# Kernel optimization log

Measured on AMD Instinct MI355X. Metric: run time of the kernel, lower is better.

Reference implementation:

```python
import jax, jax.numpy as jnp
from jax import lax
import numpy as np

EMA_ALPHA = 0.3
LN_EPS = 1e-5
SW = 5  # center_window_size


def _gelu(x):
    return jax.nn.gelu(x, approximate=False)  # torch nn.GELU default = exact erf


def _layernorm(x, g, b):
    mu = x.mean(-1, keepdims=True)
    var = ((x - mu) ** 2).mean(-1, keepdims=True)
    return (x - mu) * lax.rsqrt(var + LN_EPS) * g + b


def _ema_scan(x, alpha):
    # x: [B, T, C]; x_smooth[t] = lerp(x_smooth[t-1], x[t], alpha)
    x0 = x[:, 0]
    def step(prev, xt):
        s = prev + alpha * (xt - prev)
        return s, s
    _, ys = lax.scan(step, x0, jnp.swapaxes(x[:, 1:], 0, 1))  # [T-1, B, C]
    return jnp.concatenate([x0[:, None], jnp.swapaxes(ys, 0, 1)], axis=1)


def _lstm_dir(x, w_ih, w_hh, b):
    # x: [B, T, Cin]; w_ih: [Cin, 4H]; w_hh: [H, 4H]; b: [4H]. torch gate order i,f,g,o
    B = x.shape[0]
    H = w_hh.shape[0]
    pre = jnp.einsum('btc,ch->bth', x, w_ih) + b  # [B, T, 4H]
    def step(carry, p):
        h, c = carry
        gates = p + h @ w_hh
        i, f, g, o = jnp.split(gates, 4, axis=-1)
        c = jax.nn.sigmoid(f) * c + jax.nn.sigmoid(i) * jnp.tanh(g)
        h = jax.nn.sigmoid(o) * jnp.tanh(c)
        return (h, c), h
    init = (jnp.zeros((B, H), x.dtype), jnp.zeros((B, H), x.dtype))
    _, hs = lax.scan(step, init, jnp.swapaxes(pre, 0, 1))  # [T, B, H]
    return jnp.swapaxes(hs, 0, 1)


def _bilstm(x, wih_f, whh_f, b_f, wih_r, whh_r, b_r):
    fwd = _lstm_dir(x, wih_f, whh_f, b_f)
    bwd = jnp.flip(_lstm_dir(jnp.flip(x, axis=1), wih_r, whh_r, b_r), axis=1)
    return jnp.concatenate([fwd, bwd], axis=-1)  # [B, T, 2H]


def setup_inputs() -> dict:
    key = jax.random.key(0)
    ks = jax.random.split(key, 24)
    B, T, C, BD, O, H = 4096, 31, 768, 128, 12, 64
    AUG = 3 * BD  # 384
    def n(k, shape, s):
        return jax.random.normal(k, shape, dtype=jnp.float32) * s
    return {
        'x': n(ks[0], (B, T, C), 1.0),
        'cls_w': n(ks[1], (C, BD), 0.03), 'cls_b': jnp.zeros((BD,), jnp.float32),
        'delta_w': n(ks[2], (C, BD), 0.03), 'delta_b': jnp.zeros((BD,), jnp.float32),
        'acc_w': n(ks[3], (C, BD), 0.03), 'acc_b': jnp.zeros((BD,), jnp.float32),
        'cls_ln_g': jnp.ones((BD,), jnp.float32), 'cls_ln_b': jnp.zeros((BD,), jnp.float32),
        'delta_ln_g': jnp.ones((BD,), jnp.float32), 'delta_ln_b': jnp.zeros((BD,), jnp.float32),
        'acc_ln_g': jnp.ones((BD,), jnp.float32), 'acc_ln_b': jnp.zeros((BD,), jnp.float32),
        'lin0_w': n(ks[4], (AUG, 256), 0.05), 'lin0_b': jnp.zeros((256,), jnp.float32),
        'gate': jnp.float32(0.2),
        'attn_w': n(ks[5], (2 * H, 1), 0.08), 'attn_b': jnp.zeros((1,), jnp.float32),
        'attn_temp': jnp.float32(1.0),
        'lin1_w': n(ks[6], (C, O), 0.03), 'lin1_b': jnp.zeros((O,), jnp.float32),
        'lin2_w': n(ks[7], (2 * H, O), 0.08), 'lin2_b': jnp.zeros((O,), jnp.float32),
        'lstm_wih_f': n(ks[8], (256, 4 * H), 0.06), 'lstm_whh_f': n(ks[9], (H, 4 * H), 0.12),
        'lstm_b_f': jnp.zeros((4 * H,), jnp.float32),
        'lstm_wih_r': n(ks[10], (256, 4 * H), 0.06), 'lstm_whh_r': n(ks[11], (H, 4 * H), 0.12),
        'lstm_b_r': jnp.zeros((4 * H,), jnp.float32),
    }


def reference(x, cls_w, cls_b, delta_w, delta_b, acc_w, acc_b,
              cls_ln_g, cls_ln_b, delta_ln_g, delta_ln_b, acc_ln_g, acc_ln_b,
              lin0_w, lin0_b, gate, attn_w, attn_b, attn_temp,
              lin1_w, lin1_b, lin2_w, lin2_b,
              lstm_wih_f, lstm_whh_f, lstm_b_f, lstm_wih_r, lstm_whh_r, lstm_b_r):
    T = x.shape[1]
    hsl = T // 2
    l, r = max(0, hsl - SW), min(T, hsl + SW + 1)  # center window [10, 21) for T=31

    # --- robust deltas: EMA smoothing + reflect-padded finite differences ---
    x_smooth = _ema_scan(x, EMA_ALPHA)                       # [B, T, C]
    padded = jnp.pad(x_smooth, ((0, 0), (2, 0), (0, 0)), mode='reflect')  # [B, T+2, C]
    dx = padded[:, 1:] - padded[:, :-1]                       # [B, T+1, C]
    ddx = dx[:, 1:] - dx[:, :-1]                              # [B, T, C]
    delta_stream = dx[:, 1:]                                  # [B, T, C]
    acc_stream = ddx                                          # [B, T, C]

    # --- linear branch: mean of lin1 over center window of smoothed stream ---
    linear_logits = (x_smooth[:, l:r] @ lin1_w + lin1_b).mean(axis=1)  # [B, O]

    # --- bottlenecks (eval mode: dropout identity) + LayerNorms ---
    cls_bn = _layernorm(_gelu(x_smooth @ cls_w + cls_b), cls_ln_g, cls_ln_b)
    delta_bn = _layernorm(_gelu(delta_stream @ delta_w + delta_b), delta_ln_g, delta_ln_b)
    acc_bn = _layernorm(_gelu(acc_stream @ acc_w + acc_b), acc_ln_g, acc_ln_b)
    x_aug = jnp.concatenate([cls_bn, delta_bn, acc_bn], axis=-1)  # [B, T, 384]

    x_lstm = _gelu(x_aug @ lin0_w + lin0_b)                   # [B, T, 256]
    x_lstm = x_lstm - x_lstm.mean(axis=1, keepdims=True)      # center over time (fp32)

    # --- BiLSTM + attention pooling over center window ---
    lstm_out = _bilstm(x_lstm, lstm_wih_f, lstm_whh_f, lstm_b_f,
                       lstm_wih_r, lstm_whh_r, lstm_b_r)      # [B, T, 128]
    window = lstm_out[:, l:r]                                 # [B, W, 128]
    temp = jax.nn.softplus(attn_temp) + 0.001
    scores = (window @ attn_w + attn_b)[..., 0] / temp        # [B, W]
    attn = jax.nn.softmax(scores, axis=1)[..., None]          # [B, W, 1]
    attended = (attn * window).sum(axis=1)                    # [B, 128]
    lstm_logits = attended @ lin2_w + lin2_b                  # [B, O]

    g = jax.nn.sigmoid(gate)
    final_logits = linear_logits + g * (lstm_logits - linear_logits)
    return final_logits, attended
```

## Files before the change

### kernel.cpp

```cpp
#include <hip/hip_runtime.h>
#include <cstdint>
#include <cstddef>


typedef short s8v __attribute__((ext_vector_type(8)));
typedef float f4v __attribute__((ext_vector_type(4)));

#if defined(__has_builtin)
#if __has_builtin(__builtin_amdgcn_global_load_lds)
#define HAVE_GLL 1
#endif
#endif
#ifndef HAVE_GLL
#define HAVE_GLL 0
#endif

__device__ __forceinline__ unsigned short f2bf(float f) {
  union { float f; unsigned int u; } v; v.f = f;
  unsigned int u = v.u;
  return (unsigned short)((u + 0x7fffu + ((u >> 16) & 1u)) >> 16);
}
__device__ __forceinline__ float bf2f(unsigned short h) {
  union { unsigned int u; float f; } v; v.u = ((unsigned int)h) << 16;
  return v.f;
}
__device__ __forceinline__ float fsig(float x) {
  return __fdividef(1.f, 1.f + __expf(-x));
}
__device__ __forceinline__ float ftanh(float x) {
  return 1.f - __fdividef(2.f, 1.f + __expf(2.f * x));
}
__device__ __forceinline__ float fgelu(float x) {
  return 0.5f * x * (1.f + erff(x * 0.70710678118654752f));
}

__device__ __forceinline__ void ld_lds16(const unsigned short* g,
                                         unsigned short* ldsU, int lane) {
#if HAVE_GLL
  __builtin_amdgcn_global_load_lds(
      (__attribute__((address_space(1))) void*)(uintptr_t)(const void*)g,
      (__attribute__((address_space(3))) void*)(unsigned int)(uintptr_t)(void*)ldsU,
      16, 0, 0);
#else
  *(uint4*)(ldsU + lane * 8) = *(const uint4*)g;
#endif
}
__device__ __forceinline__ void wait_vm0() {
#if HAVE_GLL
  __builtin_amdgcn_s_waitcnt(0x0F70);
#endif
}

#define OFF_W1T   0u
#define OFF_W2T   589824u
#define OFF_WIHT  786432u
#define OFF_WHHT  1048576u
#define OFF_XS    1114112u
#define OFF_XW    196149248u
#define OFF_LL    208732160u
#define OFF_WIN   208928768u
#define OFF_XAUG  220463104u
#define OFF_XLSTM 317980672u

__global__ __launch_bounds__(256) void k0_prep(
    const float* __restrict__ cls_w, const float* __restrict__ delta_w,
    const float* __restrict__ acc_w, const float* __restrict__ lin0_w,
    const float* __restrict__ wih_f, const float* __restrict__ wih_r,
    const float* __restrict__ whh_f, const float* __restrict__ whh_r,
    unsigned short* __restrict__ ws) {
  int i = blockIdx.x * 256 + threadIdx.x;
  if (i < 294912) {
    int n = i / 768, k = i - n * 768;
    int seg = n >> 7, nn = n & 127;
    const float* w = seg == 0 ? cls_w : (seg == 1 ? delta_w : acc_w);
    ws[i] = f2bf(w[k * 128 + nn]);
  } else if (i < 393216) {
    int j = i - 294912;
    int n = j / 384, k = j - n * 384;
    ws[i] = f2bf(lin0_w[k * 256 + n]);
  } else if (i < 524288) {
    int j = i - 393216;
    int n = j >> 8, k = j & 255;
    ws[i] = f2bf(n < 256 ? wih_f[k * 256 + n] : wih_r[k * 256 + (n - 256)]);
  } else if (i < 557056) {
    int j = i - 524288;
    int d = j >> 14, rem = j & 16383;
    int n = rem >> 6, k = rem & 63;
    const float* w = d ? whh_r : whh_f;
    ws[i] = f2bf(w[k * 256 + n]);
  }
}

__global__ __launch_bounds__(256) void k1_ema(
    const float* __restrict__ x, unsigned short* __restrict__ xs,
    float* __restrict__ xw) {
  int gid = blockIdx.x * 256 + threadIdx.x;
  int b = gid / 768;
  int c = gid - b * 768;
  size_t base = (size_t)b * 31 * 768 + c;
  float s = x[base];
  xs[base] = f2bf(s);
  float wsum = 0.f;
#pragma unroll
  for (int t = 1; t < 31; ++t) {
    float xv = x[base + t * 768];
    s = s + 0.3f * (xv - s);
    xs[base + t * 768] = f2bf(s);
    if (t >= 10 && t <= 20) wsum += s;
  }
  xw[gid] = wsum * (1.f / 11.f);
}

__global__ __launch_bounds__(64) void k1b_linlog(
    const float* __restrict__ xw, const float* __restrict__ lin1_w,
    const float* __restrict__ lin1_b, float* __restrict__ ll) {
  int b = blockIdx.x;
  int lane = threadIdx.x;
  float p[12];
#pragma unroll
  for (int o = 0; o < 12; ++o) p[o] = 0.f;
  for (int k = lane; k < 768; k += 64) {
    float xv = xw[b * 768 + k];
    const float* w = lin1_w + k * 12;
#pragma unroll
    for (int o = 0; o < 12; ++o) p[o] += xv * w[o];
  }
#pragma unroll
  for (int o = 0; o < 12; ++o) {
    float v = p[o];
#pragma unroll
    for (int s = 1; s < 64; s <<= 1) v += __shfl_xor(v, s, 64);
    p[o] = v;
  }
  if (lane == 0) {
#pragma unroll
    for (int o = 0; o < 12; ++o) ll[b * 12 + o] = p[o] + lin1_b[o];
  }
}

template <int KDIM>
__device__ __forceinline__ void gemm128(
    const unsigned short* __restrict__ A, int rowClamp,
    const unsigned short* __restrict__ Bt,
    unsigned short* sA, unsigned short* sB, f4v acc[4][4]) {
  const int tid  = threadIdx.x;
  const int lane = tid & 63;
  const int wv   = tid >> 6;
  const int l15  = lane & 15;
  const int quad = lane >> 4;
  const int mh   = (wv >> 1) * 64;
  const int nh   = (wv & 1) * 64;

  const int srow = wv * 32 + (lane >> 3);
  const int scol = (lane & 7) * 8;
  const unsigned short* aBase[4];
  const unsigned short* bBase[4];
  unsigned short* aDst[4];
  unsigned short* bDst[4];
#pragma unroll
  for (int j = 0; j < 4; ++j) {
    int r = srow + j * 8;
    int ar = r < rowClamp ? r : rowClamp;
    aBase[j] = A + (size_t)ar * KDIM + scol;
    bBase[j] = Bt + (size_t)r * KDIM + scol;
    aDst[j] = sA + (wv * 4 + j) * 512;
    bDst[j] = sB + (wv * 4 + j) * 512;
  }
#pragma unroll
  for (int mt = 0; mt < 4; ++mt)
#pragma unroll
    for (int nt = 0; nt < 4; ++nt)
      acc[mt][nt] = (f4v){0.f, 0.f, 0.f, 0.f};

  constexpr int KT = KDIM / 64;
  for (int kt = 0; kt < KT; ++kt) {
    if (kt) __syncthreads();
    int ko = kt * 64;
#pragma unroll
    for (int j = 0; j < 4; ++j) ld_lds16(aBase[j] + ko, aDst[j], lane);
#pragma unroll
    for (int j = 0; j < 4; ++j) ld_lds16(bBase[j] + ko, bDst[j], lane);
    wait_vm0();
    __syncthreads();
#pragma unroll
    for (int ks = 0; ks < 2; ++ks) {
      s8v af[4], bfv[4];
#pragma unroll
      for (int mt = 0; mt < 4; ++mt)
        af[mt] = *(const s8v*)(&sA[(mh + mt * 16 + l15) * 64 + ks * 32 + quad * 8]);
#pragma unroll
      for (int nt = 0; nt < 4; ++nt)
        bfv[nt] = *(const s8v*)(&sB[(nh + nt * 16 + l15) * 64 + ks * 32 + quad * 8]);
#pragma unroll
      for (int mt = 0; mt < 4; ++mt)
#pragma unroll
        for (int nt = 0; nt < 4; ++nt)
          acc[mt][nt] = __builtin_amdgcn_mfma_f32_16x16x32_bf16(af[mt], bfv[nt], acc[mt][nt], 0, 0, 0);
    }
  }
  __syncthreads();
}

__device__ __forceinline__ void dump_chunk(f4v acc[4][4], float* sP, int lo,
                                           int nrows, int pstr) {
  const int tid  = threadIdx.x;
  const int lane = tid & 63;
  const int wv   = tid >> 6;
  const int l15  = lane & 15;
  const int quad = lane >> 4;
  const int mh   = (wv >> 1) * 64;
  const int nh   = (wv & 1) * 64;
#pragma unroll
  for (int mt = 0; mt < 4; ++mt)
#pragma unroll
    for (int nt = 0; nt < 4; ++nt)
#pragma unroll
      for (int r = 0; r < 4; ++r) {
        int rr = mh + mt * 16 + quad * 4 + r - lo;
        if ((unsigned)rr < (unsigned)nrows)
          sP[rr * pstr + nh + nt * 16 + l15] = acc[mt][nt][r];
      }
}

__device__ __forceinline__ float stencil_gelu3(const float* sP, const float* sBias,
                                               int seg, int t, int c) {
  const float* p = sP + t * 390 + seg * 130 + c;
  float v;
  if (seg == 0) {
    v = p[0];
  } else if (seg == 1) {
    v = (t == 0) ? (p[0] - p[390]) : (p[0] - p[-390]);
  } else {
    if (t == 0)      v = p[0] - 2.f * p[390] + p[780];
    else if (t == 1) v = 2.f * (p[0] - p[-390]);
    else             v = p[0] - 2.f * p[-390] + p[-780];
  }
  return fgelu(v + sBias[seg * 128 + c]);
}

__global__ __launch_bounds__(1024) void k2_aug(
    const unsigned short* __restrict__ xs, const unsigned short* __restrict__ W1t,
    const float* __restrict__ cls_b, const float* __restrict__ delta_b,
    const float* __restrict__ acc_b,
    const float* __restrict__ g0, const float* __restrict__ be0,
    const float* __restrict__ g1, const float* __restrict__ be1,
    const float* __restrict__ g2, const float* __restrict__ be2,
    unsigned short* __restrict__ xaug) {
  __shared__ __align__(16) char smem[131072];
  unsigned short* buf0 = (unsigned short*)smem;
  unsigned short* buf1 = (unsigned short*)(smem + 65536);
  float* sP    = (float*)smem;
  float* sBias = (float*)(smem + 65536);
  float* sG    = sBias + 384;
  float* sLb   = sG + 384;
  float* sMu   = sLb + 384;
  float* sRs   = sMu + 93;

  const int tid  = threadIdx.x;
  const int lane = tid & 63;
  const int wv   = tid >> 6;
  const int l15  = lane & 15;
  const int quad = lane >> 4;
  const int wm   = wv >> 3;
  const int wn   = wv & 7;
  const int rowBase = blockIdx.x * 124;

  const int subrow = lane >> 3;
  const int schunk = ((lane & 7) ^ subrow) * 8;
  const unsigned short* src[4];
#pragma unroll
  for (int j = 0; j < 4; ++j) {
    int slice = wv * 4 + j;
    int row = slice * 8 + subrow;
    src[j] = (row < 128)
        ? xs + (size_t)(rowBase + (row < 124 ? row : 123)) * 768 + schunk
        : W1t + (size_t)(row - 128) * 768 + schunk;
  }

  f4v acc[4][3];
#pragma unroll
  for (int mt = 0; mt < 4; ++mt)
#pragma unroll
    for (int nt = 0; nt < 3; ++nt) acc[mt][nt] = (f4v){0.f, 0.f, 0.f, 0.f};

  const int swz = (l15 & 7) << 3;

#pragma unroll
  for (int j = 0; j < 4; ++j) ld_lds16(src[j], buf0 + (wv * 4 + j) * 512, lane);
  wait_vm0();
  __syncthreads();

  for (int kt = 0; kt < 12; ++kt) {
    unsigned short* bc = (kt & 1) ? buf1 : buf0;
    unsigned short* bn = (kt & 1) ? buf0 : buf1;
    if (kt < 11) {
#pragma unroll
      for (int j = 0; j < 4; ++j)
        ld_lds16(src[j] + (kt + 1) * 64, bn + (wv * 4 + j) * 512, lane);
    }
#pragma unroll
    for (int ks = 0; ks < 2; ++ks) {
      s8v af[4], bfv[3];
      const int ko = (ks * 32 + quad * 8) ^ swz;
#pragma unroll
      for (int mt = 0; mt < 4; ++mt)
        af[mt] = *(const s8v*)(&bc[(wm * 64 + mt * 16 + l15) * 64 + ko]);
#pragma unroll
      for (int nt = 0; nt < 3; ++nt)
        bfv[nt] = *(const s8v*)(&bc[(128 + wn * 48 + nt * 16 + l15) * 64 + ko]);
#pragma unroll
      for (int mt = 0; mt < 4; ++mt)
#pragma unroll
        for (int nt = 0; nt < 3; ++nt)
          acc[mt][nt] = __builtin_amdgcn_mfma_f32_16x16x32_bf16(af[mt], bfv[nt], acc[mt][nt], 0, 0, 0);
    }
    wait_vm0();
    __syncthreads();
  }

  if (tid < 384) {
    int seg = tid >> 7, c = tid & 127;
    sBias[tid] = seg == 0 ? cls_b[c] : (seg == 1 ? delta_b[c] : acc_b[c]);
    sG[tid]    = seg == 0 ? g0[c]    : (seg == 1 ? g1[c]    : g2[c]);
    sLb[tid]   = seg == 0 ? be0[c]   : (seg == 1 ? be1[c]   : be2[c]);
  }

#pragma unroll
  for (int ck = 0; ck < 4; ++ck) {
    int lo = ck * 31;
#pragma unroll
    for (int mt = 0; mt < 4; ++mt) {
      int rbase = wm * 64 + mt * 16 + quad * 4 - lo;
#pragma unroll
      for (int nt = 0; nt < 3; ++nt) {
        int gcol = wn * 48 + nt * 16;
        int colp = (gcol >> 7) * 130 + (gcol & 127) + l15;
#pragma unroll
        for (int r = 0; r < 4; ++r) {
          int rr = rbase + r;
          if ((unsigned)rr < 31u) sP[rr * 390 + colp] = acc[mt][nt][r];
        }
      }
    }
    __syncthreads();
    if (tid < 744) {
      int seg = tid < 248 ? 0 : (tid < 496 ? 1 : 2);
      int rem = tid - seg * 248;
      int row = rem >> 3, q = rem & 7;
      float sum = 0.f, ss = 0.f;
#pragma unroll
      for (int i = 0; i < 16; ++i) {
        float v = stencil_gelu3(sP, sBias, seg, row, q + 8 * i);
        sum += v; ss += v * v;
      }
      sum += __shfl_xor(sum, 1, 64); ss += __shfl_xor(ss, 1, 64);
      sum += __shfl_xor(sum, 2, 64); ss += __shfl_xor(ss, 2, 64);
      sum += __shfl_xor(sum, 4, 64); ss += __shfl_xor(ss, 4, 64);
      if (q == 0) {
        float mu = sum * (1.f / 128.f);
        sMu[seg * 31 + row] = mu;
        sRs[seg * 31 + row] = rsqrtf(ss * (1.f / 128.f) - mu * mu + 1e-5f);
      }
    }
    __syncthreads();
#pragma unroll
    for (int seg = 0; seg < 3; ++seg) {
      for (int idx = tid; idx < 31 * 128; idx += 1024) {
        int row = idx >> 7, c = idx & 127;
        float v = stencil_gelu3(sP, sBias, seg, row, c);
        float o = (v - sMu[seg * 31 + row]) * sRs[seg * 31 + row]
                  * sG[seg * 128 + c] + sLb[seg * 128 + c];
        xaug[(size_t)(rowBase + lo + row) * 384 + seg * 128 + c] = f2bf(o);
      }
    }
    __syncthreads();
  }
}

__global__ __launch_bounds__(256) void k3_lstm_in(
    const unsigned short* __restrict__ xaug, const unsigned short* __restrict__ W2t,
    const float* __restrict__ lin0_b, unsigned short* __restrict__ xlstm) {
  __shared__ __align__(16) char smem[33792];
  unsigned short* sA = (unsigned short*)smem;
  unsigned short* sB = (unsigned short*)(smem + 16384);
  float* sP  = (float*)smem;
  float* sCM = (float*)(smem + 32768);
  int by = blockIdx.y;
  int rowBase = blockIdx.x * 124;
  f4v acc[4][4];
  gemm128<384>(xaug + (size_t)rowBase * 384, 123, W2t + (size_t)by * 128 * 384, sA, sB, acc);
  int tid = threadIdx.x;
#pragma unroll
  for (int ck = 0; ck < 2; ++ck) {
    int lo = ck * 62;
    dump_chunk(acc, sP, lo, 62, 132);
    __syncthreads();
    for (int idx = tid; idx < 62 * 128; idx += 256) {
      int row = idx >> 7, col = idx & 127;
      sP[row * 132 + col] = fgelu(sP[row * 132 + col] + lin0_b[by * 128 + col]);
    }
    __syncthreads();
    {
      int bb = tid >> 7, col = tid & 127;
      float s = 0.f;
      for (int tr = 0; tr < 31; ++tr) s += sP[(bb * 31 + tr) * 132 + col];
      sCM[tid] = s * (1.f / 31.f);
    }
    __syncthreads();
    for (int idx = tid; idx < 62 * 128; idx += 256) {
      int row = idx >> 7, col = idx & 127;
      int bb = row >= 31 ? 1 : 0;
      float v = sP[row * 132 + col] - sCM[bb * 128 + col];
      xlstm[(size_t)(rowBase + lo + row) * 256 + by * 128 + col] = f2bf(v);
    }
    __syncthreads();
  }
}

__global__ __launch_bounds__(256) void k3b_pre(
    const unsigned short* __restrict__ xlstm, const unsigned short* __restrict__ Wiht,
    const float* __restrict__ b_f, const float* __restrict__ b_r,
    unsigned short* __restrict__ pre) {
  __shared__ __align__(16) char smem[32768];
  unsigned short* sA = (unsigned short*)smem;
  unsigned short* sB = (unsigned short*)(smem + 16384);
  float* sP = (float*)smem;
  int by = blockIdx.y;
  int rowBase = blockIdx.x * 128;
  f4v acc[4][4];
  gemm128<256>(xlstm + (size_t)rowBase * 256, 127, Wiht + (size_t)by * 128 * 256, sA, sB, acc);
  int tid = threadIdx.x;
#pragma unroll
  for (int ck = 0; ck < 2; ++ck) {
    int lo = ck * 64;
    dump_chunk(acc, sP, lo, 64, 128);
    __syncthreads();
    for (int idx = tid; idx < 64 * 128; idx += 256) {
      int row = idx >> 7, col = idx & 127;
      int gcol = by * 128 + col;
      float bias = gcol < 256 ? b_f[gcol] : b_r[gcol - 256];
      pre[(size_t)(rowBase + lo + row) * 512 + gcol] = f2bf(sP[row * 128 + col] + bias);
    }
    __syncthreads();
  }
}

__global__ __launch_bounds__(256) void k4_lstm(
    const unsigned short* __restrict__ pre, const unsigned short* __restrict__ Whht,
    unsigned short* __restrict__ win) {
  __shared__ unsigned short sW[256 * 72];
  __shared__ unsigned short sH[16 * 72];
  __shared__ float sG[16 * 260];
  int tid = threadIdx.x;
  int dir = blockIdx.y;
  int b0  = blockIdx.x * 16;
  {
    const unsigned short* src = Whht + dir * 16384;
#pragma unroll
    for (int c = 0; c < 8; ++c) {
      int id = tid + c * 256;
      int row = id >> 3, kc = (id & 7) * 8;
      uint4 v = *(const uint4*)(src + row * 64 + kc);
      *(uint4*)(&sW[row * 72 + kc]) = v;
    }
  }
  for (int i = tid; i < 16 * 72; i += 256) sH[i] = 0;
  __syncthreads();

  const int lane = tid & 63, wv = tid >> 6, l15 = lane & 15, quad = lane >> 4;
  const int eb = tid >> 4, jb = (tid & 15) * 4;
  float cs[4] = {0.f, 0.f, 0.f, 0.f};

  int tt0 = dir ? 30 : 0;
  const unsigned short* pbase = pre + ((size_t)(b0 + eb) * 31) * 512 + dir * 256;
  ushort4 pi = *(const ushort4*)(pbase + tt0 * 512 + jb);
  ushort4 pf = *(const ushort4*)(pbase + tt0 * 512 + 64 + jb);
  ushort4 pg = *(const ushort4*)(pbase + tt0 * 512 + 128 + jb);
  ushort4 po = *(const ushort4*)(pbase + tt0 * 512 + 192 + jb);

  for (int t = 0; t < 31; ++t) {
    f4v acc[4];
#pragma unroll
    for (int nt = 0; nt < 4; ++nt) acc[nt] = (f4v){0.f, 0.f, 0.f, 0.f};
#pragma unroll
    for (int ks = 0; ks < 2; ++ks) {
      s8v af = *(const s8v*)(&sH[l15 * 72 + ks * 32 + quad * 8]);
#pragma unroll
      for (int nt = 0; nt < 4; ++nt) {
        int n = wv * 64 + nt * 16 + l15;
        s8v bfv = *(const s8v*)(&sW[n * 72 + ks * 32 + quad * 8]);
        acc[nt] = __builtin_amdgcn_mfma_f32_16x16x32_bf16(af, bfv, acc[nt], 0, 0, 0);
      }
    }
#pragma unroll
    for (int nt = 0; nt < 4; ++nt)
#pragma unroll
      for (int r = 0; r < 4; ++r)
        sG[(quad * 4 + r) * 260 + wv * 64 + nt * 16 + l15] = acc[nt][r];

    ushort4 ni, nf, ng, no;
    if (t < 30) {
      int ttn = dir ? 29 - t : t + 1;
      ni = *(const ushort4*)(pbase + ttn * 512 + jb);
      nf = *(const ushort4*)(pbase + ttn * 512 + 64 + jb);
      ng = *(const ushort4*)(pbase + ttn * 512 + 128 + jb);
      no = *(const ushort4*)(pbase + ttn * 512 + 192 + jb);
    }
    __syncthreads();

    int tt = dir ? 30 - t : t;
    const float* g = &sG[eb * 260];
    float hv[4];
#pragma unroll
    for (int jj = 0; jj < 4; ++jj) {
      int j = jb + jj;
      float vi = g[j]       + bf2f(jj == 0 ? pi.x : jj == 1 ? pi.y : jj == 2 ? pi.z : pi.w);
      float vf = g[64 + j]  + bf2f(jj == 0 ? pf.x : jj == 1 ? pf.y : jj == 2 ? pf.z : pf.w);
      float vg = g[128 + j] + bf2f(jj == 0 ? pg.x : jj == 1 ? pg.y : jj == 2 ? pg.z : pg.w);
      float vo = g[192 + j] + bf2f(jj == 0 ? po.x : jj == 1 ? po.y : jj == 2 ? po.z : po.w);
      float cc = fsig(vf) * cs[jj] + fsig(vi) * ftanh(vg);
      cs[jj] = cc;
      hv[jj] = fsig(vo) * ftanh(cc);
    }
    ushort4 hb;
    hb.x = f2bf(hv[0]); hb.y = f2bf(hv[1]); hb.z = f2bf(hv[2]); hb.w = f2bf(hv[3]);
    *(ushort4*)(&sH[eb * 72 + jb]) = hb;
    if (tt >= 10 && tt <= 20)
      *(ushort4*)(win + ((size_t)(b0 + eb) * 11 + (tt - 10)) * 128 + dir * 64 + jb) = hb;
    if (t < 30) { pi = ni; pf = nf; pg = ng; po = no; }
    __syncthreads();
  }
}

__global__ __launch_bounds__(256) void k5_attn(
    const unsigned short* __restrict__ win, const float* __restrict__ attn_w,
    const float* __restrict__ attn_b, const float* __restrict__ attn_t,
    const float* __restrict__ lin2_w, const float* __restrict__ lin2_b,
    const float* __restrict__ linlog, const float* __restrict__ gate,
    float* __restrict__ out) {
  __shared__ unsigned short sWin[176 * 128];
  __shared__ float sAw[128];
  __shared__ float sSc[176];
  __shared__ float sAtt[16 * 128];
  int tid = threadIdx.x;
  int b0  = blockIdx.x * 16;
#pragma unroll
  for (int c = 0; c < 11; ++c) {
    int id = tid + c * 256;
    int row = id >> 4, kc = (id & 15) * 8;
    uint4 v = *(const uint4*)(win + ((size_t)b0 * 11 + row) * 128 + kc);
    *(uint4*)(&sWin[row * 128 + kc]) = v;
  }
  if (tid < 128) sAw[tid] = attn_w[tid];
  __syncthreads();
  if (tid < 176) {
    int b = tid / 11, wt = tid - b * 11;
    const unsigned short* w = &sWin[(b * 11 + wt) * 128];
    float dot = 0.f;
    for (int ch = 0; ch < 128; ++ch) dot += bf2f(w[ch]) * sAw[ch];
    float temp = logf(1.f + __expf(attn_t[0])) + 0.001f;
    sSc[tid] = (dot + attn_b[0]) / temp;
  }
  __syncthreads();
  if (tid < 16) {
    float m = -1e30f;
    for (int wt = 0; wt < 11; ++wt) m = fmaxf(m, sSc[tid * 11 + wt]);
    float e[11], sum = 0.f;
    for (int wt = 0; wt < 11; ++wt) { e[wt] = __expf(sSc[tid * 11 + wt] - m); sum += e[wt]; }
    float inv = __fdividef(1.f, sum);
    for (int wt = 0; wt < 11; ++wt) sSc[tid * 11 + wt] = e[wt] * inv;
  }
  __syncthreads();
#pragma unroll
  for (int p = 0; p < 8; ++p) {
    int task = tid + p * 256;
    int b = task >> 7, ch = task & 127;
    float a = 0.f;
    for (int wt = 0; wt < 11; ++wt)
      a += sSc[b * 11 + wt] * bf2f(sWin[(b * 11 + wt) * 128 + ch]);
    sAtt[b * 128 + ch] = a;
    out[49152 + (size_t)(b0 + b) * 128 + ch] = a;
  }
  __syncthreads();
  if (tid < 192) {
    int b = tid / 12, o = tid - b * 12;
    float dot = 0.f;
    for (int ch = 0; ch < 128; ++ch) dot += sAtt[b * 128 + ch] * lin2_w[ch * 12 + o];
    dot += lin2_b[o];
    float lin = linlog[(size_t)(b0 + b) * 12 + o];
    float gg = fsig(gate[0]);
    out[(size_t)(b0 + b) * 12 + o] = lin + gg * (dot - lin);
  }
}

extern "C" void kernel_launch(void* const* d_in, const int* in_sizes, int n_in,
                              void* d_out, int out_size, void* d_ws, size_t ws_size,
                              hipStream_t stream) {
  const float* x       = (const float*)d_in[0];
  const float* cls_w   = (const float*)d_in[1];
  const float* cls_b   = (const float*)d_in[2];
  const float* delta_w = (const float*)d_in[3];
  const float* delta_b = (const float*)d_in[4];
  const float* acc_w   = (const float*)d_in[5];
  const float* acc_b   = (const float*)d_in[6];
  const float* cls_g   = (const float*)d_in[7];
  const float* cls_be  = (const float*)d_in[8];
  const float* del_g   = (const float*)d_in[9];
  const float* del_be  = (const float*)d_in[10];
  const float* accg    = (const float*)d_in[11];
  const float* accbe   = (const float*)d_in[12];
  const float* lin0_w  = (const float*)d_in[13];
  const float* lin0_b  = (const float*)d_in[14];
  const float* gate    = (const float*)d_in[15];
  const float* attn_w  = (const float*)d_in[16];
  const float* attn_b  = (const float*)d_in[17];
  const float* attn_t  = (const float*)d_in[18];
  const float* lin1_w  = (const float*)d_in[19];
  const float* lin1_b  = (const float*)d_in[20];
  const float* lin2_w  = (const float*)d_in[21];
  const float* lin2_b  = (const float*)d_in[22];
  const float* wih_f   = (const float*)d_in[23];
  const float* whh_f   = (const float*)d_in[24];
  const float* b_f     = (const float*)d_in[25];
  const float* wih_r   = (const float*)d_in[26];
  const float* whh_r   = (const float*)d_in[27];
  const float* b_r     = (const float*)d_in[28];

  char* ws = (char*)d_ws;
  unsigned short* W1t   = (unsigned short*)(ws + OFF_W1T);
  unsigned short* W2t   = (unsigned short*)(ws + OFF_W2T);
  unsigned short* Wiht  = (unsigned short*)(ws + OFF_WIHT);
  unsigned short* Whht  = (unsigned short*)(ws + OFF_WHHT);
  unsigned short* XS    = (unsigned short*)(ws + OFF_XS);
  unsigned short* PRE   = XS;
  float*          XW    = (float*)(ws + OFF_XW);
  float*          LL    = (float*)(ws + OFF_LL);
  unsigned short* WIN   = (unsigned short*)(ws + OFF_WIN);
  unsigned short* XAUG  = (unsigned short*)(ws + OFF_XAUG);
  unsigned short* XLSTM = (unsigned short*)(ws + OFF_XLSTM);
  float* out = (float*)d_out;

  k0_prep<<<2176, 256, 0, stream>>>(cls_w, delta_w, acc_w, lin0_w, wih_f, wih_r,
                                    whh_f, whh_r, (unsigned short*)ws);
  k1_ema<<<12288, 256, 0, stream>>>(x, XS, XW);
  k1b_linlog<<<4096, 64, 0, stream>>>(XW, lin1_w, lin1_b, LL);
  k2_aug<<<1024, 1024, 0, stream>>>(XS, W1t, cls_b, delta_b, acc_b,
                                    cls_g, cls_be, del_g, del_be, accg, accbe, XAUG);
  k3_lstm_in<<<dim3(1024, 2), 256, 0, stream>>>(XAUG, W2t, lin0_b, XLSTM);
  k3b_pre<<<dim3(992, 4), 256, 0, stream>>>(XLSTM, Wiht, b_f, b_r, PRE);
  k4_lstm<<<dim3(256, 2), 256, 0, stream>>>(PRE, Whht, WIN);
  k5_attn<<<256, 256, 0, stream>>>(WIN, attn_w, attn_b, attn_t, lin2_w, lin2_b,
                                   LL, gate, out);
}
```

Baseline: 1.101 ms.

## Fuse lin0 GEMM, centering and LSTM input projection into one kernel

Merges the lin0+GELU+time-centering kernel and the LSTM input-projection kernel into a single 1024-thread kernel. The centered activations stay in LDS instead of round-tripping through global memory. The GEMM tiles are double-buffered with XOR-swizzled LDS layouts so loads overlap MFMA work. The EMA kernel is also changed to process two channels per thread with float2 loads and packed bf16 stores. The fused kernel needs about 132KB of LDS and 1024 threads per block, which limits occupancy to one block per CU.

```diff
diff --git a/kernel.cpp b/kernel.cpp
--- a/kernel.cpp
+++ b/kernel.cpp
@@ -60,7 +60,6 @@
 #define OFF_LL    208732160u
 #define OFF_WIN   208928768u
 #define OFF_XAUG  220463104u
-#define OFF_XLSTM 317980672u
 
 __global__ __launch_bounds__(256) void k0_prep(
     const float* __restrict__ cls_w, const float* __restrict__ delta_w,
@@ -95,20 +94,24 @@
     const float* __restrict__ x, unsigned short* __restrict__ xs,
     float* __restrict__ xw) {
   int gid = blockIdx.x * 256 + threadIdx.x;
-  int b = gid / 768;
-  int c = gid - b * 768;
-  size_t base = (size_t)b * 31 * 768 + c;
-  float s = x[base];
-  xs[base] = f2bf(s);
-  float wsum = 0.f;
+  int b = gid / 384;
+  int cp = gid - b * 384;
+  size_t base = (size_t)b * 31 * 768 + cp * 2;
+  float2 s = *(const float2*)(x + base);
+  *(unsigned int*)(xs + base) =
+      (unsigned int)f2bf(s.x) | ((unsigned int)f2bf(s.y) << 16);
+  float w0 = 0.f, w1 = 0.f;
 #pragma unroll
   for (int t = 1; t < 31; ++t) {
-    float xv = x[base + t * 768];
-    s = s + 0.3f * (xv - s);
-    xs[base + t * 768] = f2bf(s);
-    if (t >= 10 && t <= 20) wsum += s;
-  }
-  xw[gid] = wsum * (1.f / 11.f);
+    float2 xv = *(const float2*)(x + base + t * 768);
+    s.x += 0.3f * (xv.x - s.x);
+    s.y += 0.3f * (xv.y - s.y);
+    *(unsigned int*)(xs + base + t * 768) =
+        (unsigned int)f2bf(s.x) | ((unsigned int)f2bf(s.y) << 16);
+    if (t >= 10 && t <= 20) { w0 += s.x; w1 += s.y; }
+  }
+  float2 wm; wm.x = w0 * (1.f / 11.f); wm.y = w1 * (1.f / 11.f);
+  *(float2*)(xw + (size_t)b * 768 + cp * 2) = wm;
 }
 
 __global__ __launch_bounds__(64) void k1b_linlog(
@@ -136,90 +139,6 @@
 #pragma unroll
     for (int o = 0; o < 12; ++o) ll[b * 12 + o] = p[o] + lin1_b[o];
   }
-}
-
-template <int KDIM>
-__device__ __forceinline__ void gemm128(
-    const unsigned short* __restrict__ A, int rowClamp,
-    const unsigned short* __restrict__ Bt,
-    unsigned short* sA, unsigned short* sB, f4v acc[4][4]) {
-  const int tid  = threadIdx.x;
-  const int lane = tid & 63;
-  const int wv   = tid >> 6;
-  const int l15  = lane & 15;
-  const int quad = lane >> 4;
-  const int mh   = (wv >> 1) * 64;
-  const int nh   = (wv & 1) * 64;
-
-  const int srow = wv * 32 + (lane >> 3);
-  const int scol = (lane & 7) * 8;
-  const unsigned short* aBase[4];
-  const unsigned short* bBase[4];
-  unsigned short* aDst[4];
-  unsigned short* bDst[4];
-#pragma unroll
-  for (int j = 0; j < 4; ++j) {
-    int r = srow + j * 8;
-    int ar = r < rowClamp ? r : rowClamp;
-    aBase[j] = A + (size_t)ar * KDIM + scol;
-    bBase[j] = Bt + (size_t)r * KDIM + scol;
-    aDst[j] = sA + (wv * 4 + j) * 512;
-    bDst[j] = sB + (wv * 4 + j) * 512;
-  }
-#pragma unroll
-  for (int mt = 0; mt < 4; ++mt)
-#pragma unroll
-    for (int nt = 0; nt < 4; ++nt)
-      acc[mt][nt] = (f4v){0.f, 0.f, 0.f, 0.f};
-
-  constexpr int KT = KDIM / 64;
-  for (int kt = 0; kt < KT; ++kt) {
-    if (kt) __syncthreads();
-    int ko = kt * 64;
-#pragma unroll
-    for (int j = 0; j < 4; ++j) ld_lds16(aBase[j] + ko, aDst[j], lane);
-#pragma unroll
-    for (int j = 0; j < 4; ++j) ld_lds16(bBase[j] + ko, bDst[j], lane);
-    wait_vm0();
-    __syncthreads();
-#pragma unroll
-    for (int ks = 0; ks < 2; ++ks) {
-      s8v af[4], bfv[4];
-#pragma unroll
-      for (int mt = 0; mt < 4; ++mt)
-        af[mt] = *(const s8v*)(&sA[(mh + mt * 16 + l15) * 64 + ks * 32 + quad * 8]);
-#pragma unroll
-      for (int nt = 0; nt < 4; ++nt)
-        bfv[nt] = *(const s8v*)(&sB[(nh + nt * 16 + l15) * 64 + ks * 32 + quad * 8]);
-#pragma unroll
-      for (int mt = 0; mt < 4; ++mt)
-#pragma unroll
-        for (int nt = 0; nt < 4; ++nt)
-          acc[mt][nt] = __builtin_amdgcn_mfma_f32_16x16x32_bf16(af[mt], bfv[nt], acc[mt][nt], 0, 0, 0);
-    }
-  }
-  __syncthreads();
-}
-
-__device__ __forceinline__ void dump_chunk(f4v acc[4][4], float* sP, int lo,
-                                           int nrows, int pstr) {
-  const int tid  = threadIdx.x;
-  const int lane = tid & 63;
-  const int wv   = tid >> 6;
-  const int l15  = lane & 15;
-  const int quad = lane >> 4;
-  const int mh   = (wv >> 1) * 64;
-  const int nh   = (wv & 1) * 64;
-#pragma unroll
-  for (int mt = 0; mt < 4; ++mt)
-#pragma unroll
-    for (int nt = 0; nt < 4; ++nt)
-#pragma unroll
-      for (int r = 0; r < 4; ++r) {
-        int rr = mh + mt * 16 + quad * 4 + r - lo;
-        if ((unsigned)rr < (unsigned)nrows)
-          sP[rr * pstr + nh + nt * 16 + l15] = acc[mt][nt][r];
-      }
 }
 
 __device__ __forceinline__ float stencil_gelu3(const float* sP, const float* sBias,
@@ -377,71 +296,191 @@
   }
 }
 
-__global__ __launch_bounds__(256) void k3_lstm_in(
+__global__ __launch_bounds__(1024) void k3c_fused(
     const unsigned short* __restrict__ xaug, const unsigned short* __restrict__ W2t,
-    const float* __restrict__ lin0_b, unsigned short* __restrict__ xlstm) {
-  __shared__ __align__(16) char smem[33792];
-  unsigned short* sA = (unsigned short*)smem;
-  unsigned short* sB = (unsigned short*)(smem + 16384);
-  float* sP  = (float*)smem;
-  float* sCM = (float*)(smem + 32768);
-  int by = blockIdx.y;
-  int rowBase = blockIdx.x * 124;
-  f4v acc[4][4];
-  gemm128<384>(xaug + (size_t)rowBase * 384, 123, W2t + (size_t)by * 128 * 384, sA, sB, acc);
-  int tid = threadIdx.x;
-#pragma unroll
-  for (int ck = 0; ck < 2; ++ck) {
-    int lo = ck * 62;
-    dump_chunk(acc, sP, lo, 62, 132);
-    __syncthreads();
-    for (int idx = tid; idx < 62 * 128; idx += 256) {
-      int row = idx >> 7, col = idx & 127;
-      sP[row * 132 + col] = fgelu(sP[row * 132 + col] + lin0_b[by * 128 + col]);
-    }
-    __syncthreads();
-    {
-      int bb = tid >> 7, col = tid & 127;
-      float s = 0.f;
-      for (int tr = 0; tr < 31; ++tr) s += sP[(bb * 31 + tr) * 132 + col];
-      sCM[tid] = s * (1.f / 31.f);
-    }
-    __syncthreads();
-    for (int idx = tid; idx < 62 * 128; idx += 256) {
-      int row = idx >> 7, col = idx & 127;
-      int bb = row >= 31 ? 1 : 0;
-      float v = sP[row * 132 + col] - sCM[bb * 128 + col];
-      xlstm[(size_t)(rowBase + lo + row) * 256 + by * 128 + col] = f2bf(v);
-    }
-    __syncthreads();
-  }
-}
-
-__global__ __launch_bounds__(256) void k3b_pre(
-    const unsigned short* __restrict__ xlstm, const unsigned short* __restrict__ Wiht,
+    const unsigned short* __restrict__ Wiht, const float* __restrict__ lin0_b,
     const float* __restrict__ b_f, const float* __restrict__ b_r,
     unsigned short* __restrict__ pre) {
-  __shared__ __align__(16) char smem[32768];
-  unsigned short* sA = (unsigned short*)smem;
-  unsigned short* sB = (unsigned short*)(smem + 16384);
-  float* sP = (float*)smem;
-  int by = blockIdx.y;
-  int rowBase = blockIdx.x * 128;
-  f4v acc[4][4];
-  gemm128<256>(xlstm + (size_t)rowBase * 256, 127, Wiht + (size_t)by * 128 * 256, sA, sB, acc);
-  int tid = threadIdx.x;
-#pragma unroll
-  for (int ck = 0; ck < 2; ++ck) {
-    int lo = ck * 64;
-    dump_chunk(acc, sP, lo, 64, 128);
-    __syncthreads();
-    for (int idx = tid; idx < 64 * 128; idx += 256) {
-      int row = idx >> 7, col = idx & 127;
-      int gcol = by * 128 + col;
-      float bias = gcol < 256 ? b_f[gcol] : b_r[gcol - 256];
-      pre[(size_t)(rowBase + lo + row) * 512 + gcol] = f2bf(sP[row * 128 + col] + bias);
-    }
-    __syncthreads();
+  __shared__ __align__(16) char smem[135168];
+  unsigned short* stg2  = (unsigned short*)smem;
+  unsigned short* xlstm = (unsigned short*)smem;
+  unsigned short* stg3  = (unsigned short*)(smem + 65536);
+  unsigned short* sPb   = (unsigned short*)(smem + 65536);
+  float*          sP2   = (float*)(smem + 98304);
+  float* sL0b = (float*)(smem + 131072);
+  float* sB3  = sL0b + 256;
+  float* sCM  = sB3 + 512;
+
+  const int tid  = threadIdx.x;
+  const int lane = tid & 63;
+  const int wv   = tid >> 6;
+  const int l15  = lane & 15;
+  const int quad = lane >> 4;
+  const int wm   = wv >> 3;
+  const int wn   = wv & 7;
+  const int rowBase = blockIdx.x * 124;
+
+  if (tid < 256) sL0b[tid] = lin0_b[tid];
+  else if (tid < 768) {
+    int i = tid - 256;
+    sB3[i] = i < 256 ? b_f[i] : b_r[i - 256];
+  }
+
+  const int subrow  = lane >> 3;
+  const int schunk8 = ((lane & 7) ^ subrow) * 8;
+  const int swz     = (l15 & 7) << 3;
+
+  const unsigned short* src2[3];
+#pragma unroll
+  for (int j = 0; j < 3; ++j) {
+    int row = (wv * 3 + j) * 8 + subrow;
+    src2[j] = (row < 128)
+        ? xaug + (size_t)(rowBase + (row < 124 ? row : 123)) * 384 + schunk8
+        : W2t + (size_t)(row - 128) * 384 + schunk8;
+  }
+  f4v acc2[4][2];
+#pragma unroll
+  for (int mt = 0; mt < 4; ++mt)
+#pragma unroll
+    for (int nt = 0; nt < 2; ++nt) acc2[mt][nt] = (f4v){0.f, 0.f, 0.f, 0.f};
+
+#pragma unroll
+  for (int j = 0; j < 3; ++j) ld_lds16(src2[j], stg2 + (wv * 3 + j) * 512, lane);
+  wait_vm0();
+  __syncthreads();
+
+  for (int kt = 0; kt < 6; ++kt) {
+    unsigned short* bc = stg2 + (kt & 1) * 24576;
+    unsigned short* bn = stg2 + ((kt & 1) ^ 1) * 24576;
+    if (kt < 5) {
+#pragma unroll
+      for (int j = 0; j < 3; ++j)
+        ld_lds16(src2[j] + (kt + 1) * 64, bn + (wv * 3 + j) * 512, lane);
+    }
+#pragma unroll
+    for (int ks = 0; ks < 2; ++ks) {
+      const int ko = (ks * 32 + quad * 8) ^ swz;
+      s8v af[4], bfv[2];
+#pragma unroll
+      for (int mt = 0; mt < 4; ++mt)
+        af[mt] = *(const s8v*)(&bc[(wm * 64 + mt * 16 + l15) * 64 + ko]);
+#pragma unroll
+      for (int nt = 0; nt < 2; ++nt)
+        bfv[nt] = *(const s8v*)(&bc[(128 + wn * 32 + nt * 16 + l15) * 64 + ko]);
+#pragma unroll
+      for (int mt = 0; mt < 4; ++mt)
+#pragma unroll
+        for (int nt = 0; nt < 2; ++nt)
+          acc2[mt][nt] = __builtin_amdgcn_mfma_f32_16x16x32_bf16(af[mt], bfv[nt], acc2[mt][nt], 0, 0, 0);
+    }
+    wait_vm0();
+    __syncthreads();
+  }
+
+  for (int ck = 0; ck < 4; ++ck) {
+    const int lo = ck * 31;
+#pragma unroll
+    for (int mt = 0; mt < 4; ++mt) {
+      int rbase = wm * 64 + mt * 16 + quad * 4 - lo;
+#pragma unroll
+      for (int nt = 0; nt < 2; ++nt) {
+        int col = wn * 32 + nt * 16 + l15;
+#pragma unroll
+        for (int r = 0; r < 4; ++r) {
+          int rr = rbase + r;
+          if ((unsigned)rr < 31u) sP2[rr * 260 + col] = acc2[mt][nt][r];
+        }
+      }
+    }
+    __syncthreads();
+    for (int idx = tid; idx < 31 * 256; idx += 1024) {
+      int row = idx >> 8, col = idx & 255;
+      sP2[row * 260 + col] = fgelu(sP2[row * 260 + col] + sL0b[col]);
+    }
+    __syncthreads();
+    if (tid < 256) {
+      float s = 0.f;
+      for (int tr = 0; tr < 31; ++tr) s += sP2[tr * 260 + tid];
+      sCM[tid] = s * (1.f / 31.f);
+    }
+    __syncthreads();
+    for (int idx = tid; idx < 31 * 128; idx += 1024) {
+      int row = idx >> 7, cp = (idx & 127) * 2;
+      float v0 = sP2[row * 260 + cp]     - sCM[cp];
+      float v1 = sP2[row * 260 + cp + 1] - sCM[cp + 1];
+      unsigned int u = (unsigned int)f2bf(v0) | ((unsigned int)f2bf(v1) << 16);
+      *(unsigned int*)(&xlstm[(size_t)(lo + row) * 260 + cp]) = u;
+    }
+    __syncthreads();
+  }
+
+  for (int p = 0; p < 2; ++p) {
+    const unsigned short* src3[2];
+#pragma unroll
+    for (int j = 0; j < 2; ++j) {
+      int row = (wv * 2 + j) * 8 + subrow;
+      src3[j] = Wiht + (size_t)(p * 256 + row) * 256 + schunk8;
+    }
+    f4v acc3[4][2];
+#pragma unroll
+    for (int mt = 0; mt < 4; ++mt)
+#pragma unroll
+      for (int nt = 0; nt < 2; ++nt) acc3[mt][nt] = (f4v){0.f, 0.f, 0.f, 0.f};
+#pragma unroll
+    for (int j = 0; j < 2; ++j) ld_lds16(src3[j], stg3 + (wv * 2 + j) * 512, lane);
+    wait_vm0();
+    __syncthreads();
+    for (int kt = 0; kt < 4; ++kt) {
+      unsigned short* bc = stg3 + (kt & 1) * 16384;
+      unsigned short* bn = stg3 + ((kt & 1) ^ 1) * 16384;
+      if (kt < 3) {
+#pragma unroll
+        for (int j = 0; j < 2; ++j)
+          ld_lds16(src3[j] + (kt + 1) * 64, bn + (wv * 2 + j) * 512, lane);
+      }
+#pragma unroll
+      for (int ks = 0; ks < 2; ++ks) {
+        const int ko = (ks * 32 + quad * 8) ^ swz;
+        s8v af[4], bfv[2];
+#pragma unroll
+        for (int mt = 0; mt < 4; ++mt)
+          af[mt] = *(const s8v*)(&xlstm[(size_t)(wm * 64 + mt * 16 + l15) * 260 + kt * 64 + ks * 32 + quad * 8]);
+#pragma unroll
+        for (int nt = 0; nt < 2; ++nt)
+          bfv[nt] = *(const s8v*)(&bc[(wn * 32 + nt * 16 + l15) * 64 + ko]);
+#pragma unroll
+        for (int mt = 0; mt < 4; ++mt)
+#pragma unroll
+          for (int nt = 0; nt < 2; ++nt)
+            acc3[mt][nt] = __builtin_amdgcn_mfma_f32_16x16x32_bf16(af[mt], bfv[nt], acc3[mt][nt], 0, 0, 0);
+      }
+      wait_vm0();
+      __syncthreads();
+    }
+    for (int ck = 0; ck < 4; ++ck) {
+      const int lo = ck * 31;
+#pragma unroll
+      for (int mt = 0; mt < 4; ++mt) {
+        int rbase = wm * 64 + mt * 16 + quad * 4 - lo;
+#pragma unroll
+        for (int nt = 0; nt < 2; ++nt) {
+          int col = wn * 32 + nt * 16 + l15;
+          float bias = sB3[p * 256 + col];
+#pragma unroll
+          for (int r = 0; r < 4; ++r) {
+            int rr = rbase + r;
+            if ((unsigned)rr < 31u) sPb[rr * 264 + col] = f2bf(acc3[mt][nt][r] + bias);
+          }
+        }
+      }
+      __syncthreads();
+      if (tid < 992) {
+        int row = tid >> 5, cq = (tid & 31) * 8;
+        *(uint4*)(pre + (size_t)(rowBase + lo + row) * 512 + p * 256 + cq) =
+            *(const uint4*)(&sPb[row * 264 + cq]);
+      }
+      __syncthreads();
+    }
   }
 }
 
@@ -637,17 +676,15 @@
   float*          LL    = (float*)(ws + OFF_LL);
   unsigned short* WIN   = (unsigned short*)(ws + OFF_WIN);
   unsigned short* XAUG  = (unsigned short*)(ws + OFF_XAUG);
-  unsigned short* XLSTM = (unsigned short*)(ws + OFF_XLSTM);
   float* out = (float*)d_out;
 
   k0_prep<<<2176, 256, 0, stream>>>(cls_w, delta_w, acc_w, lin0_w, wih_f, wih_r,
                                     whh_f, whh_r, (unsigned short*)ws);
-  k1_ema<<<12288, 256, 0, stream>>>(x, XS, XW);
+  k1_ema<<<6144, 256, 0, stream>>>(x, XS, XW);
   k1b_linlog<<<4096, 64, 0, stream>>>(XW, lin1_w, lin1_b, LL);
   k2_aug<<<1024, 1024, 0, stream>>>(XS, W1t, cls_b, delta_b, acc_b,
                                     cls_g, cls_be, del_g, del_be, accg, accbe, XAUG);
-  k3_lstm_in<<<dim3(1024, 2), 256, 0, stream>>>(XAUG, W2t, lin0_b, XLSTM);
-  k3b_pre<<<dim3(992, 4), 256, 0, stream>>>(XLSTM, Wiht, b_f, b_r, PRE);
+  k3c_fused<<<1024, 1024, 0, stream>>>(XAUG, W2t, Wiht, lin0_b, b_f, b_r, PRE);
   k4_lstm<<<dim3(256, 2), 256, 0, stream>>>(PRE, Whht, WIN);
   k5_attn<<<256, 256, 0, stream>>>(WIN, attn_w, attn_b, attn_t, lin2_w, lin2_b,
                                    LL, gate, out);
```

New measurement: 1.180 ms. 1.07x slower.

## Restructure LSTM recurrence to per-wave batches and vectorize EMA loads

Applied to the files above, without the earlier changes.

The LSTM kernel now gives each wavefront its own 16-row batch and has it compute all 256 gate columns. Gate nonlinearities are applied directly on MFMA accumulators, which removes the shared gate buffer and both block-wide barriers per timestep. The hidden state is exchanged through a per-wave LDS slot with only a waitcnt, and the precomputed input gates seed the accumulators. Separately, the EMA kernel processes four channels per thread with float4 loads, cutting its grid by four. In exchange, the LSTM uses more registers per thread (16 accumulators plus prefetch buffers), which can lower occupancy, and it launches half as many blocks of 128 threads.

```diff
diff --git a/kernel.cpp b/kernel.cpp
--- a/kernel.cpp
+++ b/kernel.cpp
@@ -95,20 +95,27 @@
     const float* __restrict__ x, unsigned short* __restrict__ xs,
     float* __restrict__ xw) {
   int gid = blockIdx.x * 256 + threadIdx.x;
-  int b = gid / 768;
-  int c = gid - b * 768;
-  size_t base = (size_t)b * 31 * 768 + c;
-  float s = x[base];
-  xs[base] = f2bf(s);
-  float wsum = 0.f;
+  int b = gid / 192;
+  int cq = gid - b * 192;
+  size_t base = (size_t)b * 31 * 768 + cq * 4;
+  float4 s = *(const float4*)(x + base);
+  ushort4 o;
+  o.x = f2bf(s.x); o.y = f2bf(s.y); o.z = f2bf(s.z); o.w = f2bf(s.w);
+  *(ushort4*)(xs + base) = o;
+  float w0 = 0.f, w1 = 0.f, w2 = 0.f, w3 = 0.f;
 #pragma unroll
   for (int t = 1; t < 31; ++t) {
-    float xv = x[base + t * 768];
-    s = s + 0.3f * (xv - s);
-    xs[base + t * 768] = f2bf(s);
-    if (t >= 10 && t <= 20) wsum += s;
-  }
-  xw[gid] = wsum * (1.f / 11.f);
+    float4 xv = *(const float4*)(x + base + t * 768);
+    s.x += 0.3f * (xv.x - s.x); s.y += 0.3f * (xv.y - s.y);
+    s.z += 0.3f * (xv.z - s.z); s.w += 0.3f * (xv.w - s.w);
+    o.x = f2bf(s.x); o.y = f2bf(s.y); o.z = f2bf(s.z); o.w = f2bf(s.w);
+    *(ushort4*)(xs + base + t * 768) = o;
+    if (t >= 10 && t <= 20) { w0 += s.x; w1 += s.y; w2 += s.z; w3 += s.w; }
+  }
+  float4 wm;
+  wm.x = w0 * (1.f / 11.f); wm.y = w1 * (1.f / 11.f);
+  wm.z = w2 * (1.f / 11.f); wm.w = w3 * (1.f / 11.f);
+  *(float4*)(xw + (size_t)b * 768 + cq * 4) = wm;
 }
 
 __global__ __launch_bounds__(64) void k1b_linlog(
@@ -445,90 +452,111 @@
   }
 }
 
-__global__ __launch_bounds__(256) void k4_lstm(
+__global__ __launch_bounds__(128) void k4_lstm(
     const unsigned short* __restrict__ pre, const unsigned short* __restrict__ Whht,
     unsigned short* __restrict__ win) {
   __shared__ unsigned short sW[256 * 72];
-  __shared__ unsigned short sH[16 * 72];
-  __shared__ float sG[16 * 260];
-  int tid = threadIdx.x;
-  int dir = blockIdx.y;
-  int b0  = blockIdx.x * 16;
+  __shared__ unsigned short sH[2][16 * 72];
+  const int tid  = threadIdx.x;
+  const int dir  = blockIdx.x & 1;
+  const int bg   = blockIdx.x >> 1;
+  const int wv   = tid >> 6;
+  const int lane = tid & 63;
+  const int l15  = lane & 15;
+  const int quad = lane >> 4;
+  const int b0   = bg * 32 + wv * 16;
+
   {
     const unsigned short* src = Whht + dir * 16384;
-#pragma unroll
-    for (int c = 0; c < 8; ++c) {
-      int id = tid + c * 256;
+    for (int id = tid; id < 2048; id += 128) {
       int row = id >> 3, kc = (id & 7) * 8;
-      uint4 v = *(const uint4*)(src + row * 64 + kc);
-      *(uint4*)(&sW[row * 72 + kc]) = v;
-    }
-  }
-  for (int i = tid; i < 16 * 72; i += 256) sH[i] = 0;
+      *(uint4*)(&sW[row * 72 + kc]) = *(const uint4*)(src + row * 64 + kc);
+    }
+  }
+  for (int i = lane; i < 16 * 72; i += 64) sH[wv][i] = 0;
   __syncthreads();
 
-  const int lane = tid & 63, wv = tid >> 6, l15 = lane & 15, quad = lane >> 4;
-  const int eb = tid >> 4, jb = (tid & 15) * 4;
-  float cs[4] = {0.f, 0.f, 0.f, 0.f};
-
-  int tt0 = dir ? 30 : 0;
-  const unsigned short* pbase = pre + ((size_t)(b0 + eb) * 31) * 512 + dir * 256;
-  ushort4 pi = *(const ushort4*)(pbase + tt0 * 512 + jb);
-  ushort4 pf = *(const ushort4*)(pbase + tt0 * 512 + 64 + jb);
-  ushort4 pg = *(const ushort4*)(pbase + tt0 * 512 + 128 + jb);
-  ushort4 po = *(const ushort4*)(pbase + tt0 * 512 + 192 + jb);
+  const unsigned short* pb[4];
+#pragma unroll
+  for (int r = 0; r < 4; ++r)
+    pb[r] = pre + ((size_t)(b0 + quad * 4 + r) * 31) * 512 + dir * 256 + l15;
+
+  float cs[4][4];
+#pragma unroll
+  for (int nt = 0; nt < 4; ++nt)
+#pragma unroll
+    for (int r = 0; r < 4; ++r) cs[nt][r] = 0.f;
+
+  s8v hf0 = {0, 0, 0, 0, 0, 0, 0, 0};
+  s8v hf1 = {0, 0, 0, 0, 0, 0, 0, 0};
+
+  unsigned short pcur[16][4];
+  {
+    const int tt0 = dir ? 30 : 0;
+#pragma unroll
+    for (int nt = 0; nt < 16; ++nt)
+#pragma unroll
+      for (int r = 0; r < 4; ++r)
+        pcur[nt][r] = pb[r][(size_t)tt0 * 512 + nt * 16];
+  }
 
   for (int t = 0; t < 31; ++t) {
-    f4v acc[4];
-#pragma unroll
-    for (int nt = 0; nt < 4; ++nt) acc[nt] = (f4v){0.f, 0.f, 0.f, 0.f};
+    const int tt = dir ? 30 - t : t;
+    f4v acc[16];
+#pragma unroll
+    for (int nt = 0; nt < 16; ++nt)
+#pragma unroll
+      for (int r = 0; r < 4; ++r) acc[nt][r] = bf2f(pcur[nt][r]);
+
+    unsigned short pnext[16][4];
+    if (t < 30) {
+      const int ttn = dir ? 29 - t : t + 1;
+#pragma unroll
+      for (int nt = 0; nt < 16; ++nt)
+#pragma unroll
+        for (int r = 0; r < 4; ++r)
+          pnext[nt][r] = pb[r][(size_t)ttn * 512 + nt * 16];
+    }
+
 #pragma unroll
     for (int ks = 0; ks < 2; ++ks) {
-      s8v af = *(const s8v*)(&sH[l15 * 72 + ks * 32 + quad * 8]);
-#pragma unroll
-      for (int nt = 0; nt < 4; ++nt) {
-        int n = wv * 64 + nt * 16 + l15;
-        s8v bfv = *(const s8v*)(&sW[n * 72 + ks * 32 + quad * 8]);
+      s8v af = ks ? hf1 : hf0;
+#pragma unroll
+      for (int nt = 0; nt < 16; ++nt) {
+        s8v bfv = *(const s8v*)(&sW[(nt * 16 + l15) * 72 + ks * 32 + quad * 8]);
         acc[nt] = __builtin_amdgcn_mfma_f32_16x16x32_bf16(af, bfv, acc[nt], 0, 0, 0);
       }
     }
+
+    const bool wwin = (tt >= 10 && tt <= 20);
 #pragma unroll
     for (int nt = 0; nt < 4; ++nt)
 #pragma unroll
-      for (int r = 0; r < 4; ++r)
-        sG[(quad * 4 + r) * 260 + wv * 64 + nt * 16 + l15] = acc[nt][r];
-
-    ushort4 ni, nf, ng, no;
+      for (int r = 0; r < 4; ++r) {
+        float vi = acc[nt][r],     vf = acc[nt + 4][r];
+        float vg = acc[nt + 8][r], vo = acc[nt + 12][r];
+        float cc = fsig(vf) * cs[nt][r] + fsig(vi) * ftanh(vg);
+        cs[nt][r] = cc;
+        float hv = fsig(vo) * ftanh(cc);
+        unsigned short hb = f2bf(hv);
+        sH[wv][(quad * 4 + r) * 72 + nt * 16 + l15] = hb;
+        if (wwin)
+          win[((size_t)(b0 + quad * 4 + r) * 11 + (tt - 10)) * 128
+              + dir * 64 + nt * 16 + l15] = hb;
+      }
+
+    __builtin_amdgcn_sched_barrier(0);
+    asm volatile("s_waitcnt lgkmcnt(0)" ::: "memory");
+    __builtin_amdgcn_sched_barrier(0);
+    hf0 = *(const s8v*)(&sH[wv][l15 * 72 + quad * 8]);
+    hf1 = *(const s8v*)(&sH[wv][l15 * 72 + 32 + quad * 8]);
+
     if (t < 30) {
-      int ttn = dir ? 29 - t : t + 1;
-      ni = *(const ushort4*)(pbase + ttn * 512 + jb);
-      nf = *(const ushort4*)(pbase + ttn * 512 + 64 + jb);
-      ng = *(const ushort4*)(pbase + ttn * 512 + 128 + jb);
-      no = *(const ushort4*)(pbase + ttn * 512 + 192 + jb);
-    }
-    __syncthreads();
-
-    int tt = dir ? 30 - t : t;
-    const float* g = &sG[eb * 260];
-    float hv[4];
-#pragma unroll
-    for (int jj = 0; jj < 4; ++jj) {
-      int j = jb + jj;
-      float vi = g[j]       + bf2f(jj == 0 ? pi.x : jj == 1 ? pi.y : jj == 2 ? pi.z : pi.w);
-      float vf = g[64 + j]  + bf2f(jj == 0 ? pf.x : jj == 1 ? pf.y : jj == 2 ? pf.z : pf.w);
-      float vg = g[128 + j] + bf2f(jj == 0 ? pg.x : jj == 1 ? pg.y : jj == 2 ? pg.z : pg.w);
-      float vo = g[192 + j] + bf2f(jj == 0 ? po.x : jj == 1 ? po.y : jj == 2 ? po.z : po.w);
-      float cc = fsig(vf) * cs[jj] + fsig(vi) * ftanh(vg);
-      cs[jj] = cc;
-      hv[jj] = fsig(vo) * ftanh(cc);
-    }
-    ushort4 hb;
-    hb.x = f2bf(hv[0]); hb.y = f2bf(hv[1]); hb.z = f2bf(hv[2]); hb.w = f2bf(hv[3]);
-    *(ushort4*)(&sH[eb * 72 + jb]) = hb;
-    if (tt >= 10 && tt <= 20)
-      *(ushort4*)(win + ((size_t)(b0 + eb) * 11 + (tt - 10)) * 128 + dir * 64 + jb) = hb;
-    if (t < 30) { pi = ni; pf = nf; pg = ng; po = no; }
-    __syncthreads();
+#pragma unroll
+      for (int nt = 0; nt < 16; ++nt)
+#pragma unroll
+        for (int r = 0; r < 4; ++r) pcur[nt][r] = pnext[nt][r];
+    }
   }
 }
 
@@ -642,13 +670,13 @@
 
   k0_prep<<<2176, 256, 0, stream>>>(cls_w, delta_w, acc_w, lin0_w, wih_f, wih_r,
                                     whh_f, whh_r, (unsigned short*)ws);
-  k1_ema<<<12288, 256, 0, stream>>>(x, XS, XW);
+  k1_ema<<<3072, 256, 0, stream>>>(x, XS, XW);
   k1b_linlog<<<4096, 64, 0, stream>>>(XW, lin1_w, lin1_b, LL);
   k2_aug<<<1024, 1024, 0, stream>>>(XS, W1t, cls_b, delta_b, acc_b,
                                     cls_g, cls_be, del_g, del_be, accg, accbe, XAUG);
   k3_lstm_in<<<dim3(1024, 2), 256, 0, stream>>>(XAUG, W2t, lin0_b, XLSTM);
   k3b_pre<<<dim3(992, 4), 256, 0, stream>>>(XLSTM, Wiht, b_f, b_r, PRE);
-  k4_lstm<<<dim3(256, 2), 256, 0, stream>>>(PRE, Whht, WIN);
+  k4_lstm<<<256, 128, 0, stream>>>(PRE, Whht, WIN);
   k5_attn<<<256, 256, 0, stream>>>(WIN, attn_w, attn_b, attn_t, lin2_w, lin2_b,
                                    LL, gate, out);
 }
```

Result: slower. 1.193 ms (+8.4%).
